# Kernel optimization log

Measured on AMD Instinct MI355X. Metric: run time of the kernel, lower is better.

## Reference

```python
import jax, jax.numpy as jnp
import numpy as np

RANGES = (1, 2, 4, 10, 25)
B, L, D, V = 64, 1000, 300, 50000  # L divisible by every r in RANGES -> no remainder group


def setup_inputs() -> dict:
    key = jax.random.key(0)
    ks = jax.random.split(key, 12)
    u = lambda k, s: jax.random.uniform(k, s, dtype=jnp.float32) / 6  # matches torch.rand(...)/6
    return {
        "article_in": jax.random.randint(ks[0], (B, L), 0, V),
        "emb": jax.random.normal(ks[1], (V, D), dtype=jnp.float32) * 0.02,
        "w_ce": u(ks[2], (len(RANGES), D, D)),   # per-range W in contract-expand
        "b_ce": u(ks[3], (len(RANGES), 1, D)),   # per-range b (shape (1,D) in source)
        "w1": u(ks[4], (3, len(RANGES))),
        "b1": u(ks[5], (3, D)),
        "w2": u(ks[6], (1, 3)),
        "b2": u(ks[7], (1, D)),
        "wz": u(ks[8], (D, D)),
        "bz": u(ks[9], (1, D)),
        "wo": u(ks[10], (D, D)),
        "bo": u(ks[11], (1, D)),
    }


def _mru(x, w_ce, b_ce, w1, b1, w2, b2, wz, bz, wo, bo):
    b, l, d = x.shape
    # --- contract-expand: segment-sum windows of size r, tiny matmul, broadcast back /r ---
    ce = []
    for i, r in enumerate(RANGES):
        seg = x.reshape(b, l // r, r, d).sum(axis=2)                 # [B, L/r, D] segment sums
        t = jax.nn.relu(seg @ w_ce[i]) + b_ce[i]                     # relu(sum @ W) + b
        ce.append(jnp.repeat(t, r, axis=1) / r)                      # expand each group back, divided by r
    pre = jnp.stack(ce, axis=2)                                      # [B, L, 5, D]
    # --- multi-ranged reasoning MLP across the 5 ranges ---
    h1 = jax.nn.relu(jnp.einsum('ts,blsd->bltd', w1, pre) + b1)      # [B, L, 3, D]
    gate = jax.nn.relu(jnp.einsum('ot,bltd->blod', w2, h1) + b2)[:, :, 0, :]  # [B, L, D]
    # --- gated recurrent encoding (note: bias added OUTSIDE tanh, per source) ---
    z = jnp.tanh(x @ wz) + bz                                        # [B, L, D]
    o = jnp.tanh(x @ wo) + bo                                        # [B, L, D]

    def step(c, inp):
        g, zt, ot = inp
        c = g * c + (1.0 - g) * zt
        return c, ot * c

    seq = (gate.transpose(1, 0, 2), z.transpose(1, 0, 2), o.transpose(1, 0, 2))  # [L, B, D]
    _, h = jax.lax.scan(step, jnp.zeros((b, d), x.dtype), seq)
    return h.transpose(1, 0, 2)                                      # [B, L, D]


def reference(article_in, emb, w_ce, b_ce, w1, b1, w2, b2, wz, bz, wo, bo):
    x = emb[article_in]                                              # embedding lookup [B, L, D]
    return _mru(x, w_ce, b_ce, w1, b1, w2, b2, wz, bz, wo, bo)
```

## Files before the change

### kernel.cpp

```cpp
#include <hip/hip_runtime.h>
#include <hip/hip_bf16.h>

typedef unsigned short u16;
typedef unsigned int   u32;
typedef __attribute__((ext_vector_type(8))) short short8;
typedef __attribute__((ext_vector_type(4))) float floatx4;
typedef __attribute__((ext_vector_type(4))) unsigned short u16x4;

__device__ __forceinline__ u16 f2bf(float f){
  u32 x = __float_as_uint(f);
  u32 r = (x + 0x7fffu + ((x >> 16) & 1u)) >> 16;
  return (u16)r;
}
__device__ __forceinline__ float bf2f(u16 u){
  return __uint_as_float(((u32)u) << 16);
}
__device__ __forceinline__ float tanh_fast(float x){
  float xs = fminf(fmaxf(x, -16.f), 16.f);
  float e  = __builtin_amdgcn_exp2f(xs * 2.8853900817779268f);
  return (e - 1.f) * __builtin_amdgcn_rcpf(e + 1.f);
}
__device__ __forceinline__ void gload16(const void* g, void* l){
  __builtin_amdgcn_global_load_lds(
      (const __attribute__((address_space(1))) unsigned int*)g,
      (__attribute__((address_space(3))) unsigned int*)l, 16, 0, 0);
}

__global__ void k_gather_seg(const int* __restrict__ idx, const float* __restrict__ emb,
                             u16* __restrict__ x, u16* __restrict__ s2,
                             u16* __restrict__ s4, u16* __restrict__ s10, int total){
  int i = blockIdx.x * blockDim.x + threadIdx.x;
  if (i >= total) return;
  int d4 = i % 80; int rest = i / 80; int w = rest % 50; int b = rest / 50;
  const int dcol = d4 * 4;
  const int r0 = b * 1000 + w * 20;
  float a2[4] = {0,0,0,0}, a4[4] = {0,0,0,0}, a10[4] = {0,0,0,0};
  #pragma unroll
  for (int j = 0; j < 20; j++){
    const int r = r0 + j;
    u16x4 o; o[0] = 0; o[1] = 0; o[2] = 0; o[3] = 0;
    if (d4 < 75){
      const float4 v = *(const float4*)(emb + (size_t)idx[r] * 300 + dcol);
      o[0] = f2bf(v.x); o[1] = f2bf(v.y); o[2] = f2bf(v.z); o[3] = f2bf(v.w);
      a2[0] += v.x; a2[1] += v.y; a2[2] += v.z; a2[3] += v.w;
      a4[0] += v.x; a4[1] += v.y; a4[2] += v.z; a4[3] += v.w;
      a10[0] += v.x; a10[1] += v.y; a10[2] += v.z; a10[3] += v.w;
    }
    *(u16x4*)(x + (size_t)r * 320 + dcol) = o;
    if (j & 1){
      u16x4 s; 
      #pragma unroll
      for (int q = 0; q < 4; q++){ s[q] = f2bf(a2[q]); a2[q] = 0.f; }
      *(u16x4*)(s2 + ((size_t)(b * 500 + w * 10 + (j >> 1)) * 320 + dcol)) = s;
    }
    if ((j & 3) == 3){
      u16x4 s;
      #pragma unroll
      for (int q = 0; q < 4; q++){ s[q] = f2bf(a4[q]); a4[q] = 0.f; }
      *(u16x4*)(s4 + ((size_t)(b * 250 + w * 5 + (j >> 2)) * 320 + dcol)) = s;
    }
    if (j == 9 || j == 19){
      u16x4 s;
      #pragma unroll
      for (int q = 0; q < 4; q++){ s[q] = f2bf(a10[q]); a10[q] = 0.f; }
      *(u16x4*)(s10 + ((size_t)(b * 100 + w * 2 + j / 10) * 320 + dcol)) = s;
    }
  }
}

__global__ void k_s25(const u16* __restrict__ x, u16* __restrict__ s25, int total){
  int i = blockIdx.x * blockDim.x + threadIdx.x;
  if (i >= total) return;
  int d4 = i % 80; int rest = i / 80; int g = rest % 40; int b = rest / 40;
  const int dcol = d4 * 4;
  const u16* src = x + ((size_t)(b * 1000 + g * 25) * 320 + dcol);
  float a[4] = {0,0,0,0};
  #pragma unroll
  for (int j = 0; j < 25; j++){
    u16x4 v = *(const u16x4*)(src + (size_t)j * 320);
    #pragma unroll
    for (int q = 0; q < 4; q++) a[q] += bf2f(v[q]);
  }
  u16x4 o;
  #pragma unroll
  for (int q = 0; q < 4; q++) o[q] = f2bf(a[q]);
  *(u16x4*)(s25 + ((size_t)(b * 40 + g) * 320 + dcol)) = o;
}

__global__ void k_wprep(const float* __restrict__ wce, const float* __restrict__ wz,
                        const float* __restrict__ wo, u16* __restrict__ wT, int total){
  int i = blockIdx.x * blockDim.x + threadIdx.x;
  if (i >= total) return;
  int mat = i / 102400; int rem = i - mat * 102400;
  int n = rem / 320;    int k = rem - n * 320;
  float v = 0.f;
  if (n < 300 && k < 300){
    const float* src = (mat < 5) ? (wce + mat * 90000) : (mat == 5 ? wz : wo);
    v = src[k * 300 + n];
  }
  wT[i] = f2bf(v);
}

__global__ __launch_bounds__(256, 3) void k_gemm_all(
    const u16* __restrict__ x,  const u16* __restrict__ s2,
    const u16* __restrict__ s4, const u16* __restrict__ s10,
    const u16* __restrict__ s25,const u16* __restrict__ wT,
    u16* __restrict__ t0, u16* __restrict__ t1, u16* __restrict__ t2,
    u16* __restrict__ t3, u16* __restrict__ t4,
    u16* __restrict__ zb, u16* __restrict__ ob,
    const float* __restrict__ b_ce, const float* __restrict__ bz,
    const float* __restrict__ bo)
{
  __shared__ __align__(16) char lds[49152];

  const int bid = blockIdx.x;
  const u16 *A, *BT; u16* C; const float* bias;
  int mode; float scale; long tileRow;
  if (bid < 3000){
    const int xcd = bid & 7, j = bid >> 3;
    const int T = (j / 3) * 8 + xcd, m = j % 3;
    tileRow = (long)T * 64; A = x;
    if (m == 0)      { BT = wT;              C = t0; bias = b_ce; mode = 0; scale = 1.f; }
    else if (m == 1) { BT = wT + 5 * 102400; C = zb; bias = bz;   mode = 1; scale = 1.f; }
    else             { BT = wT + 6 * 102400; C = ob; bias = bo;   mode = 1; scale = 1.f; }
  } else {
    const int g = bid - 3000;
    if (g < 500)      { A=s2;  BT=wT+1*102400; C=t1; bias=b_ce+300;  mode=0; scale=0.5f;  tileRow=(long)g*64; }
    else if (g < 750) { A=s4;  BT=wT+2*102400; C=t2; bias=b_ce+600;  mode=0; scale=0.25f; tileRow=(long)(g-500)*64; }
    else if (g < 850) { A=s10; BT=wT+3*102400; C=t3; bias=b_ce+900;  mode=0; scale=0.1f;  tileRow=(long)(g-750)*64; }
    else              { A=s25; BT=wT+4*102400; C=t4; bias=b_ce+1200; mode=0; scale=0.04f; tileRow=(long)(g-850)*64; }
  }

  const int tid  = threadIdx.x;
  const int lane = tid & 63;
  const int wid  = tid >> 6;

  const int arow = tid >> 2, ac = tid & 3;
  const u16* aSrc = A + (tileRow + arow) * 320 + ((ac ^ ((arow >> 1) & 3)) << 3);
  const u16* bSrc[5];
  #pragma unroll
  for (int l = 0; l < 5; l++){
    const int idx2 = l * 256 + tid, col = idx2 >> 2, cc = idx2 & 3;
    bSrc[l] = BT + col * 320 + ((cc ^ ((col >> 1) & 3)) << 3);
  }
  const int wbase = wid * 1024;

  const int rA  = lane & 15;
  const int cBt = wid * 80 + (lane & 15);
  const int kchunk = ((lane >> 4) ^ ((lane >> 1) & 3)) << 4;

  floatx4 acc[4][5];
  #pragma unroll
  for (int m = 0; m < 4; m++)
    #pragma unroll
    for (int n = 0; n < 5; n++)
      #pragma unroll
      for (int q = 0; q < 4; q++) acc[m][n][q] = 0.f;

  gload16(aSrc, lds + wbase);
  #pragma unroll
  for (int l = 0; l < 5; l++) gload16(bSrc[l], lds + 8192 + l * 4096 + wbase);
  __syncthreads();

  #pragma unroll
  for (int t = 0; t < 10; t++){
    const int cur = t & 1;
    if (t < 9){
      const int nb = cur ^ 1;
      gload16(aSrc + (t + 1) * 32, lds + nb * 4096 + wbase);
      #pragma unroll
      for (int l = 0; l < 5; l++)
        gload16(bSrc[l] + (t + 1) * 32, lds + 8192 + nb * 20480 + l * 4096 + wbase);
    }
    const char* bA = lds + cur * 4096;
    const char* bB = lds + 8192 + cur * 20480;
    short8 af[4], bf[5];
    #pragma unroll
    for (int m = 0; m < 4; m++)
      af[m] = *(const short8*)(bA + (rA + m * 16) * 64 + kchunk);
    #pragma unroll
    for (int n = 0; n < 5; n++)
      bf[n] = *(const short8*)(bB + (cBt + n * 16) * 64 + kchunk);
    #pragma unroll
    for (int m = 0; m < 4; m++)
      #pragma unroll
      for (int n = 0; n < 5; n++)
        acc[m][n] = __builtin_amdgcn_mfma_f32_16x16x32_bf16(af[m], bf[n], acc[m][n], 0, 0, 0);
    __syncthreads();
  }

  const int colbase = wid * 80 + (lane & 15);
  const long rowb   = tileRow + ((lane >> 4) << 2);
  #pragma unroll
  for (int m = 0; m < 4; m++){
    #pragma unroll
    for (int n = 0; n < 5; n++){
      const int gcol = colbase + n * 16;
      if (gcol < 300){
        const float bv = bias[gcol];
        #pragma unroll
        for (int r = 0; r < 4; r++){
          const long grow = rowb + m * 16 + r;
          float v = acc[m][n][r];
          v = (mode == 0) ? (fmaxf(v, 0.f) + bv) * scale : tanh_fast(v) + bv;
          C[grow * 300 + gcol] = f2bf(v);
        }
      }
    }
  }
}

__device__ __forceinline__ float gate_eval(
    float p0, float p1, float p2, float p3, float p4,
    const float W1[3][5], const float W2[3], const float B1[3], float B2)
{
  float acc2 = B2;
  #pragma unroll
  for (int t = 0; t < 3; t++){
    float u = W1[t][0]*p0 + W1[t][1]*p1 + W1[t][2]*p2 + W1[t][3]*p3 + W1[t][4]*p4 + B1[t];
    acc2 += W2[t] * fmaxf(u, 0.f);
  }
  return fmaxf(acc2, 0.f);
}

__global__ void k_scan1(const u16* __restrict__ t0, const u16* __restrict__ t1,
    const u16* __restrict__ t2, const u16* __restrict__ t3, const u16* __restrict__ t4,
    const u16* __restrict__ z,
    const float* __restrict__ w1, const float* __restrict__ b1,
    const float* __restrict__ w2, const float* __restrict__ b2,
    float* __restrict__ cA, float* __restrict__ cB, int total)
{
  int i = blockIdx.x * blockDim.x + threadIdx.x;
  if (i >= total) return;
  int d4 = i % 75; int rest = i / 75; int ch = rest % 40; int b = rest / 40;
  const int d = d4 * 4;
  float W1[3][5], W2[3], B1[3][4], B2[4];
  #pragma unroll
  for (int t = 0; t < 3; t++){
    #pragma unroll
    for (int s = 0; s < 5; s++) W1[t][s] = w1[t * 5 + s];
    W2[t] = w2[t];
    #pragma unroll
    for (int q = 0; q < 4; q++) B1[t][q] = b1[t * 300 + d + q];
  }
  #pragma unroll
  for (int q = 0; q < 4; q++) B2[q] = b2[d + q];
  float Ac[4] = {1.f,1.f,1.f,1.f}, Bc[4] = {0.f,0.f,0.f,0.f};
  const int l0 = ch * 25;
  const u16x4 v4 = *(const u16x4*)(t4 + (size_t)(b * 40 + ch) * 300 + d);
  for (int l = l0; l < l0 + 25; l++){
    u16x4 v0 = *(const u16x4*)(t0 + (size_t)(b * 1000 + l)        * 300 + d);
    u16x4 v1 = *(const u16x4*)(t1 + (size_t)(b * 500  + (l >> 1)) * 300 + d);
    u16x4 v2 = *(const u16x4*)(t2 + (size_t)(b * 250  + (l >> 2)) * 300 + d);
    u16x4 v3 = *(const u16x4*)(t3 + (size_t)(b * 100  + l / 10)   * 300 + d);
    u16x4 vz = *(const u16x4*)(z  + (size_t)(b * 1000 + l)        * 300 + d);
    #pragma unroll
    for (int q = 0; q < 4; q++){
      float B1q[3] = {B1[0][q], B1[1][q], B1[2][q]};
      float g  = gate_eval(bf2f(v0[q]), bf2f(v1[q]), bf2f(v2[q]), bf2f(v3[q]), bf2f(v4[q]),
                           W1, W2, B1q, B2[q]);
      Ac[q] = g * Ac[q];
      Bc[q] = g * Bc[q] + (1.f - g) * bf2f(vz[q]);
    }
  }
  *(float4*)(cA + (size_t)ch * 19200 + b * 300 + d) = make_float4(Ac[0], Ac[1], Ac[2], Ac[3]);
  *(float4*)(cB + (size_t)ch * 19200 + b * 300 + d) = make_float4(Bc[0], Bc[1], Bc[2], Bc[3]);
}

__global__ void k_scan2(const float* __restrict__ cA, const float* __restrict__ cB,
                        float* __restrict__ cinit, int total){
  int i = blockIdx.x * blockDim.x + threadIdx.x;
  if (i >= total) return;
  float c = 0.f;
  for (int ch = 0; ch < 40; ch++){
    cinit[ch * 19200 + i] = c;
    c = cA[ch * 19200 + i] * c + cB[ch * 19200 + i];
  }
}

__global__ void k_scan3(const u16* __restrict__ t0, const u16* __restrict__ t1,
    const u16* __restrict__ t2, const u16* __restrict__ t3, const u16* __restrict__ t4,
    const u16* __restrict__ z, const u16* __restrict__ o,
    const float* __restrict__ cinit,
    const float* __restrict__ w1, const float* __restrict__ b1,
    const float* __restrict__ w2, const float* __restrict__ b2,
    float* __restrict__ out, int total)
{
  int i = blockIdx.x * blockDim.x + threadIdx.x;
  if (i >= total) return;
  int d4 = i % 75; int rest = i / 75; int ch = rest % 40; int b = rest / 40;
  const int d = d4 * 4;
  float W1[3][5], W2[3], B1[3][4], B2[4];
  #pragma unroll
  for (int t = 0; t < 3; t++){
    #pragma unroll
    for (int s = 0; s < 5; s++) W1[t][s] = w1[t * 5 + s];
    W2[t] = w2[t];
    #pragma unroll
    for (int q = 0; q < 4; q++) B1[t][q] = b1[t * 300 + d + q];
  }
  #pragma unroll
  for (int q = 0; q < 4; q++) B2[q] = b2[d + q];
  float c[4];
  {
    float4 ci = *(const float4*)(cinit + (size_t)ch * 19200 + b * 300 + d);
    c[0] = ci.x; c[1] = ci.y; c[2] = ci.z; c[3] = ci.w;
  }
  const int l0 = ch * 25;
  const u16x4 v4 = *(const u16x4*)(t4 + (size_t)(b * 40 + ch) * 300 + d);
  for (int l = l0; l < l0 + 25; l++){
    u16x4 v0 = *(const u16x4*)(t0 + (size_t)(b * 1000 + l)        * 300 + d);
    u16x4 v1 = *(const u16x4*)(t1 + (size_t)(b * 500  + (l >> 1)) * 300 + d);
    u16x4 v2 = *(const u16x4*)(t2 + (size_t)(b * 250  + (l >> 2)) * 300 + d);
    u16x4 v3 = *(const u16x4*)(t3 + (size_t)(b * 100  + l / 10)   * 300 + d);
    u16x4 vz = *(const u16x4*)(z  + (size_t)(b * 1000 + l)        * 300 + d);
    u16x4 vo = *(const u16x4*)(o  + (size_t)(b * 1000 + l)        * 300 + d);
    float4 res;
    #pragma unroll
    for (int q = 0; q < 4; q++){
      float B1q[3] = {B1[0][q], B1[1][q], B1[2][q]};
      float g  = gate_eval(bf2f(v0[q]), bf2f(v1[q]), bf2f(v2[q]), bf2f(v3[q]), bf2f(v4[q]),
                           W1, W2, B1q, B2[q]);
      c[q] = g * c[q] + (1.f - g) * bf2f(vz[q]);
      ((float*)&res)[q] = bf2f(vo[q]) * c[q];
    }
    *(float4*)(out + (size_t)(b * 1000 + l) * 300 + d) = res;
  }
}

extern "C" void kernel_launch(void* const* d_in, const int* in_sizes, int n_in,
                              void* d_out, int out_size, void* d_ws, size_t ws_size,
                              hipStream_t stream){
  const int*   article = (const int*)  d_in[0];
  const float* emb     = (const float*)d_in[1];
  const float* w_ce    = (const float*)d_in[2];
  const float* b_ce    = (const float*)d_in[3];
  const float* w1      = (const float*)d_in[4];
  const float* b1      = (const float*)d_in[5];
  const float* w2      = (const float*)d_in[6];
  const float* b2      = (const float*)d_in[7];
  const float* wz      = (const float*)d_in[8];
  const float* bz      = (const float*)d_in[9];
  const float* wo      = (const float*)d_in[10];
  const float* bo      = (const float*)d_in[11];
  float* out = (float*)d_out;
  char*  ws  = (char*)d_ws;

  u16* x    = (u16*)(ws + 0UL);
  u16* s2   = (u16*)(ws + 40960000UL);
  u16* s4   = (u16*)(ws + 61440000UL);
  u16* s10  = (u16*)(ws + 71680000UL);
  u16* s25  = (u16*)(ws + 75776000UL);
  u16* wT   = (u16*)(ws + 77414400UL);
  u16* t0   = (u16*)(ws + 78848000UL);
  u16* t1   = (u16*)(ws + 117248000UL);
  u16* t2   = (u16*)(ws + 136448000UL);
  u16* t3   = (u16*)(ws + 146048000UL);
  u16* t4   = (u16*)(ws + 149888000UL);
  u16* zb   = (u16*)(ws + 151424000UL);
  u16* ob   = (u16*)(ws + 189824000UL);
  float* cA = (float*)(ws + 40960000UL);
  float* cB = (float*)(ws + 44032000UL);
  float* ci = (float*)(ws + 47104000UL);
  (void)ws_size; (void)in_sizes; (void)n_in; (void)out_size;

  k_wprep     <<<2800, 256, 0, stream>>>(w_ce, wz, wo, wT, 716800);
  k_gather_seg<<<1000, 256, 0, stream>>>(article, emb, x, s2, s4, s10, 256000);
  k_s25       <<< 800, 256, 0, stream>>>(x, s25, 204800);

  k_gemm_all<<<3890, 256, 0, stream>>>(x, s2, s4, s10, s25, wT,
                                       t0, t1, t2, t3, t4, zb, ob,
                                       b_ce, bz, bo);

  k_scan1<<<750, 256, 0, stream>>>(t0, t1, t2, t3, t4, zb, w1, b1, w2, b2, cA, cB, 192000);
  k_scan2<<< 75, 256, 0, stream>>>(cA, cB, ci, 19200);
  k_scan3<<<750, 256, 0, stream>>>(t0, t1, t2, t3, t4, zb, ob, ci, w1, b1, w2, b2, out, 192000);
}
```

Measured before the change: 240.8 us.

## Enlarge GEMM tile to 128 rows with 8 waves sharing B tile in LDS

The fused GEMM kernel now uses 512-thread blocks covering 128 output rows instead of 64. Eight waves split into two row halves that share one staged copy of the weight tile, which halves per-row weight traffic into LDS and halves the block count. The cost is more LDS per block (56KB), lower occupancy bounds (2 blocks of 512), and some wasted blocks in the tail (T>=500 early return). The row-swizzle index is now computed per wave row for the A and B fragments.

```diff
diff --git a/kernel.cpp b/kernel.cpp
--- a/kernel.cpp
+++ b/kernel.cpp
@@ -48,7 +48,7 @@
     }
     *(u16x4*)(x + (size_t)r * 320 + dcol) = o;
     if (j & 1){
-      u16x4 s; 
+      u16x4 s;
       #pragma unroll
       for (int q = 0; q < 4; q++){ s[q] = f2bf(a2[q]); a2[q] = 0.f; }
       *(u16x4*)(s2 + ((size_t)(b * 500 + w * 10 + (j >> 1)) * 320 + dcol)) = s;
@@ -101,7 +101,7 @@
   wT[i] = f2bf(v);
 }
 
-__global__ __launch_bounds__(256, 3) void k_gemm_all(
+__global__ __launch_bounds__(512, 2) void k_gemm_all(
     const u16* __restrict__ x,  const u16* __restrict__ s2,
     const u16* __restrict__ s4, const u16* __restrict__ s10,
     const u16* __restrict__ s25,const u16* __restrict__ wT,
@@ -111,43 +111,49 @@
     const float* __restrict__ b_ce, const float* __restrict__ bz,
     const float* __restrict__ bo)
 {
-  __shared__ __align__(16) char lds[49152];
+  __shared__ __align__(16) char lds[57344];
 
   const int bid = blockIdx.x;
   const u16 *A, *BT; u16* C; const float* bias;
   int mode; float scale; long tileRow;
-  if (bid < 3000){
+  if (bid < 1512){
     const int xcd = bid & 7, j = bid >> 3;
     const int T = (j / 3) * 8 + xcd, m = j % 3;
-    tileRow = (long)T * 64; A = x;
+    if (T >= 500) return;
+    tileRow = (long)T * 128; A = x;
     if (m == 0)      { BT = wT;              C = t0; bias = b_ce; mode = 0; scale = 1.f; }
     else if (m == 1) { BT = wT + 5 * 102400; C = zb; bias = bz;   mode = 1; scale = 1.f; }
     else             { BT = wT + 6 * 102400; C = ob; bias = bo;   mode = 1; scale = 1.f; }
   } else {
-    const int g = bid - 3000;
-    if (g < 500)      { A=s2;  BT=wT+1*102400; C=t1; bias=b_ce+300;  mode=0; scale=0.5f;  tileRow=(long)g*64; }
-    else if (g < 750) { A=s4;  BT=wT+2*102400; C=t2; bias=b_ce+600;  mode=0; scale=0.25f; tileRow=(long)(g-500)*64; }
-    else if (g < 850) { A=s10; BT=wT+3*102400; C=t3; bias=b_ce+900;  mode=0; scale=0.1f;  tileRow=(long)(g-750)*64; }
-    else              { A=s25; BT=wT+4*102400; C=t4; bias=b_ce+1200; mode=0; scale=0.04f; tileRow=(long)(g-850)*64; }
+    const int g = bid - 1512;
+    if (g < 250)      { A=s2;  BT=wT+1*102400; C=t1; bias=b_ce+300;  mode=0; scale=0.5f;  tileRow=(long)g*128; }
+    else if (g < 375) { A=s4;  BT=wT+2*102400; C=t2; bias=b_ce+600;  mode=0; scale=0.25f; tileRow=(long)(g-250)*128; }
+    else if (g < 425) { A=s10; BT=wT+3*102400; C=t3; bias=b_ce+900;  mode=0; scale=0.1f;  tileRow=(long)(g-375)*128; }
+    else              { A=s25; BT=wT+4*102400; C=t4; bias=b_ce+1200; mode=0; scale=0.04f; tileRow=(long)(g-425)*128; }
   }
 
   const int tid  = threadIdx.x;
   const int lane = tid & 63;
   const int wid  = tid >> 6;
+  const int wr   = wid >> 2;
+  const int wc   = wid & 3;
+  const int L    = lane & 15;
+  const int kc   = lane >> 4;
 
   const int arow = tid >> 2, ac = tid & 3;
   const u16* aSrc = A + (tileRow + arow) * 320 + ((ac ^ ((arow >> 1) & 3)) << 3);
-  const u16* bSrc[5];
-  #pragma unroll
-  for (int l = 0; l < 5; l++){
-    const int idx2 = l * 256 + tid, col = idx2 >> 2, cc = idx2 & 3;
+  const u16* bSrc[3];
+  #pragma unroll
+  for (int l = 0; l < 3; l++){
+    const int idx2 = l * 512 + tid, col = idx2 >> 2, cc = idx2 & 3;
     bSrc[l] = BT + col * 320 + ((cc ^ ((col >> 1) & 3)) << 3);
   }
   const int wbase = wid * 1024;
 
-  const int rA  = lane & 15;
-  const int cBt = wid * 80 + (lane & 15);
-  const int kchunk = ((lane >> 4) ^ ((lane >> 1) & 3)) << 4;
+  const int rA   = wr * 64 + L;
+  const int cB   = wc * 80 + L;
+  const int kchA = (kc ^ ((rA >> 1) & 3)) << 4;
+  const int kchB = (kc ^ ((cB >> 1) & 3)) << 4;
 
   floatx4 acc[4][5];
   #pragma unroll
@@ -157,30 +163,30 @@
       #pragma unroll
       for (int q = 0; q < 4; q++) acc[m][n][q] = 0.f;
 
-  gload16(aSrc, lds + wbase);
-  #pragma unroll
-  for (int l = 0; l < 5; l++) gload16(bSrc[l], lds + 8192 + l * 4096 + wbase);
+  #define STAGE(t, nb) do {                                                    \
+    gload16(aSrc + (t) * 32, lds + (nb) * 8192 + wbase);                       \
+    gload16(bSrc[0] + (t) * 32, lds + 16384 + (nb) * 20480 + wbase);           \
+    gload16(bSrc[1] + (t) * 32, lds + 16384 + (nb) * 20480 + 8192 + wbase);    \
+    if (tid < 256)                                                             \
+      gload16(bSrc[2] + (t) * 32, lds + 16384 + (nb) * 20480 + 16384 + wbase); \
+  } while (0)
+
+  STAGE(0, 0);
   __syncthreads();
 
   #pragma unroll
   for (int t = 0; t < 10; t++){
     const int cur = t & 1;
-    if (t < 9){
-      const int nb = cur ^ 1;
-      gload16(aSrc + (t + 1) * 32, lds + nb * 4096 + wbase);
-      #pragma unroll
-      for (int l = 0; l < 5; l++)
-        gload16(bSrc[l] + (t + 1) * 32, lds + 8192 + nb * 20480 + l * 4096 + wbase);
-    }
-    const char* bA = lds + cur * 4096;
-    const char* bB = lds + 8192 + cur * 20480;
+    if (t < 9) STAGE(t + 1, cur ^ 1);
+    const char* Ab = lds + cur * 8192;
+    const char* Bb = lds + 16384 + cur * 20480;
     short8 af[4], bf[5];
     #pragma unroll
     for (int m = 0; m < 4; m++)
-      af[m] = *(const short8*)(bA + (rA + m * 16) * 64 + kchunk);
+      af[m] = *(const short8*)(Ab + (rA + m * 16) * 64 + kchA);
     #pragma unroll
     for (int n = 0; n < 5; n++)
-      bf[n] = *(const short8*)(bB + (cBt + n * 16) * 64 + kchunk);
+      bf[n] = *(const short8*)(Bb + (cB + n * 16) * 64 + kchB);
     #pragma unroll
     for (int m = 0; m < 4; m++)
       #pragma unroll
@@ -188,9 +194,10 @@
         acc[m][n] = __builtin_amdgcn_mfma_f32_16x16x32_bf16(af[m], bf[n], acc[m][n], 0, 0, 0);
     __syncthreads();
   }
-
-  const int colbase = wid * 80 + (lane & 15);
-  const long rowb   = tileRow + ((lane >> 4) << 2);
+  #undef STAGE
+
+  const int colbase = wc * 80 + L;
+  const long rowb   = tileRow + wr * 64 + (kc << 2);
   #pragma unroll
   for (int m = 0; m < 4; m++){
     #pragma unroll
@@ -368,7 +375,7 @@
   k_gather_seg<<<1000, 256, 0, stream>>>(article, emb, x, s2, s4, s10, 256000);
   k_s25       <<< 800, 256, 0, stream>>>(x, s25, 204800);
 
-  k_gemm_all<<<3890, 256, 0, stream>>>(x, s2, s4, s10, s25, wT,
+  k_gemm_all<<<1957, 512, 0, stream>>>(x, s2, s4, s10, s25, wT,
                                        t0, t1, t2, t3, t4, zb, ob,
                                        b_ce, bz, bo);
 
```

After: 238.9 us. No clear change (-0.8%).

## Load whole K panel into LDS once and split GEMM tiles by column half

Applied to the files above, without the earlier changes.

The fused GEMM kernel now stages the full 64x320 A tile and a 160x320 B panel into LDS in one shot, replacing the double-buffered K-loop that synchronised every step. The output is split into two 160-column halves, which doubles the grid, and each wave now computes a 32x80 sub-tile. This removes the per-iteration barriers and shrinks accumulator registers, but it uses 140KB of LDS per block, so only one block fits per CU and there is less latency hiding. Loading A twice across the column halves also adds global traffic.

```diff
diff --git a/kernel.cpp b/kernel.cpp
--- a/kernel.cpp
+++ b/kernel.cpp
@@ -48,7 +48,7 @@
     }
     *(u16x4*)(x + (size_t)r * 320 + dcol) = o;
     if (j & 1){
-      u16x4 s; 
+      u16x4 s;
       #pragma unroll
       for (int q = 0; q < 4; q++){ s[q] = f2bf(a2[q]); a2[q] = 0.f; }
       *(u16x4*)(s2 + ((size_t)(b * 500 + w * 10 + (j >> 1)) * 320 + dcol)) = s;
@@ -101,7 +101,7 @@
   wT[i] = f2bf(v);
 }
 
-__global__ __launch_bounds__(256, 3) void k_gemm_all(
+__global__ __launch_bounds__(256, 1) void k_gemm_all(
     const u16* __restrict__ x,  const u16* __restrict__ s2,
     const u16* __restrict__ s4, const u16* __restrict__ s10,
     const u16* __restrict__ s25,const u16* __restrict__ wT,
@@ -111,93 +111,93 @@
     const float* __restrict__ b_ce, const float* __restrict__ bz,
     const float* __restrict__ bo)
 {
-  __shared__ __align__(16) char lds[49152];
+  __shared__ __align__(16) char lds[143360];
 
   const int bid = blockIdx.x;
   const u16 *A, *BT; u16* C; const float* bias;
-  int mode; float scale; long tileRow;
-  if (bid < 3000){
-    const int xcd = bid & 7, j = bid >> 3;
-    const int T = (j / 3) * 8 + xcd, m = j % 3;
+  int mode; float scale; long tileRow; int colBase;
+  if (bid < 6000){
+    const int xcd = bid & 7;
+    const int v   = bid >> 3;
+    const int T   = (v / 6) * 8 + xcd;
+    const int mem = v % 6;
+    const int mat = mem >> 1;
+    colBase = (mem & 1) * 160;
     tileRow = (long)T * 64; A = x;
-    if (m == 0)      { BT = wT;              C = t0; bias = b_ce; mode = 0; scale = 1.f; }
-    else if (m == 1) { BT = wT + 5 * 102400; C = zb; bias = bz;   mode = 1; scale = 1.f; }
-    else             { BT = wT + 6 * 102400; C = ob; bias = bo;   mode = 1; scale = 1.f; }
+    if (mat == 0)      { BT = wT;            C = t0; bias = b_ce; mode = 0; scale = 1.f; }
+    else if (mat == 1) { BT = wT + 5*102400; C = zb; bias = bz;   mode = 1; scale = 1.f; }
+    else               { BT = wT + 6*102400; C = ob; bias = bo;   mode = 1; scale = 1.f; }
   } else {
-    const int g = bid - 3000;
-    if (g < 500)      { A=s2;  BT=wT+1*102400; C=t1; bias=b_ce+300;  mode=0; scale=0.5f;  tileRow=(long)g*64; }
-    else if (g < 750) { A=s4;  BT=wT+2*102400; C=t2; bias=b_ce+600;  mode=0; scale=0.25f; tileRow=(long)(g-500)*64; }
-    else if (g < 850) { A=s10; BT=wT+3*102400; C=t3; bias=b_ce+900;  mode=0; scale=0.1f;  tileRow=(long)(g-750)*64; }
-    else              { A=s25; BT=wT+4*102400; C=t4; bias=b_ce+1200; mode=0; scale=0.04f; tileRow=(long)(g-850)*64; }
+    int g;
+    if (bid < 7000)      { g = bid - 6000; A=s2;  BT=wT+1*102400; C=t1; bias=b_ce+300;  mode=0; scale=0.5f;  }
+    else if (bid < 7500) { g = bid - 7000; A=s4;  BT=wT+2*102400; C=t2; bias=b_ce+600;  mode=0; scale=0.25f; }
+    else if (bid < 7700) { g = bid - 7500; A=s10; BT=wT+3*102400; C=t3; bias=b_ce+900;  mode=0; scale=0.1f;  }
+    else                 { g = bid - 7700; A=s25; BT=wT+4*102400; C=t4; bias=b_ce+1200; mode=0; scale=0.04f; }
+    tileRow = (long)(g >> 1) * 64; colBase = (g & 1) * 160;
   }
 
   const int tid  = threadIdx.x;
   const int lane = tid & 63;
   const int wid  = tid >> 6;
-
-  const int arow = tid >> 2, ac = tid & 3;
-  const u16* aSrc = A + (tileRow + arow) * 320 + ((ac ^ ((arow >> 1) & 3)) << 3);
-  const u16* bSrc[5];
-  #pragma unroll
-  for (int l = 0; l < 5; l++){
-    const int idx2 = l * 256 + tid, col = idx2 >> 2, cc = idx2 & 3;
-    bSrc[l] = BT + col * 320 + ((cc ^ ((col >> 1) & 3)) << 3);
-  }
-  const int wbase = wid * 1024;
-
-  const int rA  = lane & 15;
-  const int cBt = wid * 80 + (lane & 15);
-  const int kchunk = ((lane >> 4) ^ ((lane >> 1) & 3)) << 4;
-
-  floatx4 acc[4][5];
-  #pragma unroll
-  for (int m = 0; m < 4; m++)
+  const int L    = lane & 15;
+  const int kc   = lane >> 4;
+  const int wbase16 = wid * 64 * 16;
+
+  #pragma unroll
+  for (int i = 0; i < 10; i++){
+    const int idx = i * 256 + tid;
+    const int row = idx / 40, p = idx - row * 40;
+    const int src = (p & ~7) | ((p & 7) ^ (row & 7));
+    gload16(A + (tileRow + row) * 320 + src * 8, lds + i * 4096 + wbase16);
+  }
+  #pragma unroll
+  for (int i = 0; i < 25; i++){
+    const int idx = i * 256 + tid;
+    const int col = idx / 40, p = idx - col * 40;
+    const int src = (p & ~7) | ((p & 7) ^ (col & 7));
+    gload16(BT + (colBase + col) * 320 + src * 8, lds + 40960 + i * 4096 + wbase16);
+  }
+  __syncthreads();
+
+  const int wrm = (wid >> 1) * 32;
+  const int wcn = (wid & 1) * 80;
+
+  floatx4 acc[2][5];
+  #pragma unroll
+  for (int m = 0; m < 2; m++)
     #pragma unroll
     for (int n = 0; n < 5; n++)
       #pragma unroll
       for (int q = 0; q < 4; q++) acc[m][n][q] = 0.f;
 
-  gload16(aSrc, lds + wbase);
-  #pragma unroll
-  for (int l = 0; l < 5; l++) gload16(bSrc[l], lds + 8192 + l * 4096 + wbase);
-  __syncthreads();
-
   #pragma unroll
   for (int t = 0; t < 10; t++){
-    const int cur = t & 1;
-    if (t < 9){
-      const int nb = cur ^ 1;
-      gload16(aSrc + (t + 1) * 32, lds + nb * 4096 + wbase);
-      #pragma unroll
-      for (int l = 0; l < 5; l++)
-        gload16(bSrc[l] + (t + 1) * 32, lds + 8192 + nb * 20480 + l * 4096 + wbase);
-    }
-    const char* bA = lds + cur * 4096;
-    const char* bB = lds + 8192 + cur * 20480;
-    short8 af[4], bf[5];
-    #pragma unroll
-    for (int m = 0; m < 4; m++)
-      af[m] = *(const short8*)(bA + (rA + m * 16) * 64 + kchunk);
-    #pragma unroll
-    for (int n = 0; n < 5; n++)
-      bf[n] = *(const short8*)(bB + (cBt + n * 16) * 64 + kchunk);
-    #pragma unroll
-    for (int m = 0; m < 4; m++)
+    short8 af[2], bf[5];
+    #pragma unroll
+    for (int m = 0; m < 2; m++){
+      const int r = wrm + m * 16 + L;
+      af[m] = *(const short8*)(lds + r * 640 + (((4 * t + kc) ^ (r & 7)) << 4));
+    }
+    #pragma unroll
+    for (int n = 0; n < 5; n++){
+      const int c = wcn + n * 16 + L;
+      bf[n] = *(const short8*)(lds + 40960 + c * 640 + (((4 * t + kc) ^ (c & 7)) << 4));
+    }
+    #pragma unroll
+    for (int m = 0; m < 2; m++)
       #pragma unroll
       for (int n = 0; n < 5; n++)
         acc[m][n] = __builtin_amdgcn_mfma_f32_16x16x32_bf16(af[m], bf[n], acc[m][n], 0, 0, 0);
-    __syncthreads();
-  }
-
-  const int colbase = wid * 80 + (lane & 15);
-  const long rowb   = tileRow + ((lane >> 4) << 2);
-  #pragma unroll
-  for (int m = 0; m < 4; m++){
-    #pragma unroll
-    for (int n = 0; n < 5; n++){
-      const int gcol = colbase + n * 16;
-      if (gcol < 300){
-        const float bv = bias[gcol];
+  }
+
+  const long rowb = tileRow + wrm + (kc << 2);
+  #pragma unroll
+  for (int n = 0; n < 5; n++){
+    const int gcol = colBase + wcn + n * 16 + L;
+    if (gcol < 300){
+      const float bv = bias[gcol];
+      #pragma unroll
+      for (int m = 0; m < 2; m++){
         #pragma unroll
         for (int r = 0; r < 4; r++){
           const long grow = rowb + m * 16 + r;
@@ -368,7 +368,7 @@
   k_gather_seg<<<1000, 256, 0, stream>>>(article, emb, x, s2, s4, s10, 256000);
   k_s25       <<< 800, 256, 0, stream>>>(x, s25, 204800);
 
-  k_gemm_all<<<3890, 256, 0, stream>>>(x, s2, s4, s10, s25, wT,
+  k_gemm_all<<<7780, 256, 0, stream>>>(x, s2, s4, s10, s25, wT,
                                        t0, t1, t2, t3, t4, zb, ob,
                                        b_ce, bz, bo);
 
```

Measured after the change: 298.0 us. 23.8% more time.
